# Optimization experiments

Hardware: AMD Instinct MI355X
Metric: run time of the kernel (lower is better)

Reference implementation:

```python
import jax, jax.numpy as jnp
import numpy as np

B, T, C, H = 8, 2048, 384, 64

def setup_inputs() -> dict:
    key = jax.random.key(0)
    k1, k2, k3, k4 = jax.random.split(key, 4)
    x = jax.random.normal(k1, (B, T, C), dtype=jnp.float32)
    Wq = jax.random.normal(k2, (C, H), dtype=jnp.float32) * (C ** -0.5)
    Wk = jax.random.normal(k3, (C, H), dtype=jnp.float32) * (C ** -0.5)
    Wv = jax.random.normal(k4, (C, H), dtype=jnp.float32) * (C ** -0.5)
    return {"x": x, "Wq": Wq, "Wk": Wk, "Wv": Wv}

def reference(x, Wq, Wk, Wv):
    # x: (B, T, C); projections: (B, T, H)
    Bn, Tn, Cn = x.shape
    q = jnp.einsum('btc,ch->bth', x, Wq)
    k = jnp.einsum('btc,ch->bth', x, Wk)
    v = jnp.einsum('btc,ch->bth', x, Wv)
    # NOTE: source scales by C**-0.5 (embedding dim), not head_size**-0.5
    weights = jnp.einsum('bth,bsh->bts', q, k) * (Cn ** -0.5)  # (B, T, T)
    causal = jnp.tril(jnp.ones((Tn, Tn), dtype=bool))
    weights = jnp.where(causal, weights, -jnp.inf)
    # NOTE: source applies softmax over dim=1 (query/row axis), reproduced faithfully
    weights = jax.nn.softmax(weights, axis=1)
    # dropout omitted (eval-mode reference)
    return jnp.einsum('bts,bsh->bth', weights, v)
```

## Files before the change

kernel.cpp:

```cpp
#include <hip/hip_runtime.h>
#include <hip/hip_bf16.h>
#include <math.h>

#define Bn 8
#define Tn 2048
#define Cn 384
#define Hn 64
#define SCALE 0.051031036307982884f

using bf16x8 = __attribute__((ext_vector_type(8))) short;
using f32x4  = __attribute__((ext_vector_type(4))) float;

#define MFMA(a, b, c) __builtin_amdgcn_mfma_f32_16x16x32_bf16((a), (b), (c), 0, 0, 0)

static __device__ __forceinline__ short f2bf(float f) {
  unsigned u = __float_as_uint(f);
  u += 0x7fffu + ((u >> 16) & 1u);
  return (short)(u >> 16);
}
static __device__ __forceinline__ float bf2f(short s) {
  return __uint_as_float(((unsigned)(unsigned short)s) << 16);
}

__global__ __launch_bounds__(256) void wconv_kernel(
    const float* __restrict__ Wq, const float* __restrict__ Wk,
    const float* __restrict__ Wv, short* __restrict__ WbT) {
  int idx = blockIdx.x * 256 + threadIdx.x;
  int n = idx / 384, k = idx - n * 384;
  const float* W = (n < 64) ? Wq : (n < 128) ? Wk : Wv;
  WbT[idx] = f2bf(W[k * 64 + (n & 63)]);
}

__global__ __launch_bounds__(256) void proj_kernel(
    const float* __restrict__ x, const short* __restrict__ WbT,
    short* __restrict__ qb, short* __restrict__ kb, short* __restrict__ vT) {
  __shared__ short xs[16][392];
  __shared__ short vtile[64][20];
  const int tid = threadIdx.x;
  const int t0 = blockIdx.x * 16;
  const float* xb = x + (size_t)t0 * Cn;
  #pragma unroll
  for (int i = 0; i < 6; ++i) {
    int j = tid + i * 256;
    int row = j / 96, colv = (j - row * 96) * 4;
    float4 v = *(const float4*)(xb + row * Cn + colv);
    short4 s4; s4.x = f2bf(v.x); s4.y = f2bf(v.y); s4.z = f2bf(v.z); s4.w = f2bf(v.w);
    *(short4*)(&xs[row][colv]) = s4;
  }
  __syncthreads();
  const int w = tid >> 6, l15 = tid & 15, quad = (tid & 63) >> 4;
  f32x4 acc[3] = {};
  for (int ks = 0; ks < 12; ++ks) {
    bf16x8 a = *(const bf16x8*)(&xs[l15][ks * 32 + quad * 8]);
    #pragma unroll
    for (int cf = 0; cf < 3; ++cf) {
      bf16x8 bfr = *(const bf16x8*)(WbT + (size_t)(48 * w + 16 * cf + l15) * Cn + ks * 32 + quad * 8);
      acc[cf] = MFMA(a, bfr, acc[cf]);
    }
  }
  #pragma unroll
  for (int cf = 0; cf < 3; ++cf) {
    int cbase = 48 * w + 16 * cf, c = cbase + l15;
    #pragma unroll
    for (int r = 0; r < 4; ++r) {
      int row = t0 + quad * 4 + r;
      short val = f2bf(acc[cf][r]);
      if (cbase < 64)       qb[(size_t)row * Hn + c] = val;
      else if (cbase < 128) kb[(size_t)row * Hn + (c - 64)] = val;
      else                  vtile[c - 128][quad * 4 + r] = val;
    }
  }
  __syncthreads();
  const int b = t0 >> 11, t0l = t0 & 2047;
  int h = tid >> 2, tseg = (tid & 3) * 4;
  *(short4*)(vT + ((size_t)(b * Hn + h)) * Tn + t0l + tseg) =
      *(const short4*)(&vtile[h][tseg]);
}

__global__ __launch_bounds__(256) void colstats_kernel(
    const short* __restrict__ qb, const short* __restrict__ kb,
    float* __restrict__ L, short* __restrict__ Eb) {
  const int unit = blockIdx.x;
  const int b = unit >> 7, rem = unit & 127;
  const int j = rem >> 3, u = rem & 7;
  const int lo = (u * 33) >> 3, hi = ((u + 1) * 33) >> 3;
  const int big = 32 - j;
  const int tid = threadIdx.x, w = tid >> 6, l15 = tid & 15, quad = (tid & 63) >> 4;
  const size_t Ebase = (size_t)b * Tn * Tn;
  __shared__ float redl[64][17];

  auto run = [&](const int i, const int k0, const int k1) {
    if (k0 >= k1) return;
    const int s0 = i << 6;
    bf16x8 bk[8];
    #pragma unroll
    for (int nf = 0; nf < 4; ++nf) {
      const size_t krow = (size_t)(b * Tn + s0 + 16 * nf + l15) * Hn;
      bk[2 * nf]     = *(const bf16x8*)(kb + krow + quad * 8);
      bk[2 * nf + 1] = *(const bf16x8*)(kb + krow + 32 + quad * 8);
    }
    float l[4] = {0.f, 0.f, 0.f, 0.f};
    auto cload = [&](bf16x8& A0, bf16x8& A1, int k) {
      size_t ar = (size_t)(b * Tn + ((i + k) << 6) + 16 * w + l15) * Hn;
      A0 = *(const bf16x8*)(qb + ar + quad * 8);
      A1 = *(const bf16x8*)(qb + ar + 32 + quad * 8);
    };
    auto ccomp = [&](bf16x8 A0, bf16x8 A1, int k) {
      f32x4 sc[4] = {};
      #pragma unroll
      for (int nf = 0; nf < 4; ++nf) {
        sc[nf] = MFMA(A0, bk[2 * nf], sc[nf]);
        sc[nf] = MFMA(A1, bk[2 * nf + 1], sc[nf]);
      }
      const bool diag = (k == 0);
      const int tb = ((i + k) << 6) + 16 * w + quad * 4;
      #pragma unroll
      for (int nf = 0; nf < 4; ++nf) {
        int s = s0 + 16 * nf + l15;
        #pragma unroll
        for (int r = 0; r < 4; ++r) {
          float v = sc[nf][r] * SCALE;
          if (diag && (tb + r) < s) v = -INFINITY;
          float ev = __expf(v);
          l[nf] += ev;
          Eb[Ebase + (size_t)(tb + r) * Tn + s] = f2bf(ev);
        }
      }
    };
    bf16x8 a0A, a1A, a0B, a1B;
    cload(a0A, a1A, k0);
    int k = k0;
    while (k + 1 < k1) {
      cload(a0B, a1B, k + 1);
      ccomp(a0A, a1A, k);
      if (k + 2 < k1) cload(a0A, a1A, k + 2);
      ccomp(a0B, a1B, k + 1);
      k += 2;
    }
    if (k < k1) ccomp(a0A, a1A, k);
    __syncthreads();
    #pragma unroll
    for (int nf = 0; nf < 4; ++nf) redl[16 * nf + l15][w * 4 + quad] = l[nf];
    __syncthreads();
    if (tid < 64) {
      float ls = 0.f;
      #pragma unroll
      for (int q2 = 0; q2 < 16; ++q2) ls += redl[tid][q2];
      atomicAdd(&L[b * Tn + s0 + tid], ls);
    }
  };
  run(j, lo, min(hi, big));
  run(31 - j, max(lo, big) - big, hi - big);
}

__global__ __launch_bounds__(256) void vhat_kernel(
    const short* __restrict__ vT, const float* __restrict__ L,
    short* __restrict__ vS) {
  int gid = blockIdx.x * 256 + threadIdx.x;
  size_t base = (size_t)gid * 8;
  int b = (int)(base >> 17), s = (int)(base & 2047);
  short4 v0 = *(const short4*)(vT + base);
  short4 v1 = *(const short4*)(vT + base + 4);
  const float* Lp = L + b * Tn + s;
  float4 L0 = *(const float4*)(Lp);
  float4 L1 = *(const float4*)(Lp + 4);
  short4 r0, r1;
  r0.x = f2bf(bf2f(v0.x) / L0.x); r0.y = f2bf(bf2f(v0.y) / L0.y);
  r0.z = f2bf(bf2f(v0.z) / L0.z); r0.w = f2bf(bf2f(v0.w) / L0.w);
  r1.x = f2bf(bf2f(v1.x) / L1.x); r1.y = f2bf(bf2f(v1.y) / L1.y);
  r1.z = f2bf(bf2f(v1.z) / L1.z); r1.w = f2bf(bf2f(v1.w) / L1.w);
  *(short4*)(vS + base) = r0;
  *(short4*)(vS + base + 4) = r1;
}

__global__ __launch_bounds__(256) void outg_kernel(
    const short* __restrict__ Eb, const short* __restrict__ vS,
    float* __restrict__ out) {
  const int unit = blockIdx.x;
  const int b = unit >> 7, rem = unit & 127;
  const int j = rem >> 3, u = rem & 7;
  const int lo = (u * 33) >> 3, hi = ((u + 1) * 33) >> 3;
  const int big = 32 - j;
  const int tid = threadIdx.x, w = tid >> 6, l15 = tid & 15, quad = (tid & 63) >> 4;
  const size_t Bbase = (size_t)b * Hn * Tn;

  auto run = [&](const int tile, const int k0, const int k1) {
    if (k0 >= k1) return;
    const int tbase = (tile << 6) + 16 * w;
    const size_t Abase = (size_t)b * Tn * Tn + (size_t)(tbase + l15) * Tn;
    f32x4 acc[4] = {};
    bf16x8 aA[2], bA[8], aB[2], bB[8];
    auto load = [&](bf16x8 (&A)[2], bf16x8 (&Bf)[8], int ch) {
      const int s0 = ch << 6;
      A[0] = *(const bf16x8*)(Eb + Abase + s0 + quad * 8);
      A[1] = *(const bf16x8*)(Eb + Abase + s0 + 32 + quad * 8);
      #pragma unroll
      for (int nf = 0; nf < 4; ++nf) {
        const size_t br = Bbase + (size_t)(16 * nf + l15) * Tn + s0;
        Bf[2 * nf]     = *(const bf16x8*)(vS + br + quad * 8);
        Bf[2 * nf + 1] = *(const bf16x8*)(vS + br + 32 + quad * 8);
      }
    };
    auto comp = [&](bf16x8 (&A)[2], bf16x8 (&Bf)[8]) {
      #pragma unroll
      for (int nf = 0; nf < 4; ++nf) {
        acc[nf] = MFMA(A[0], Bf[2 * nf], acc[nf]);
        acc[nf] = MFMA(A[1], Bf[2 * nf + 1], acc[nf]);
      }
    };
    load(aA, bA, k0);
    int ch = k0;
    while (ch + 1 < k1) {
      load(aB, bB, ch + 1);
      comp(aA, bA);
      if (ch + 2 < k1) load(aA, bA, ch + 2);
      comp(aB, bB);
      ch += 2;
    }
    if (ch < k1) comp(aA, bA);
    #pragma unroll
    for (int nf = 0; nf < 4; ++nf)
      #pragma unroll
      for (int r = 0; r < 4; ++r)
        atomicAdd(&out[(size_t)(b * Tn + tbase + quad * 4 + r) * Hn + 16 * nf + l15],
                  acc[nf][r]);
  };
  run(31 - j, lo, min(hi, big));
  run(j, max(lo, big) - big, hi - big);
}

extern "C" void kernel_launch(void* const* d_in, const int* in_sizes, int n_in,
                              void* d_out, int out_size, void* d_ws, size_t ws_size,
                              hipStream_t stream) {
  const float* x  = (const float*)d_in[0];
  const float* Wq = (const float*)d_in[1];
  const float* Wk = (const float*)d_in[2];
  const float* Wv = (const float*)d_in[3];
  char* ws = (char*)d_ws;
  short* qb   = (short*)(ws);
  short* kb   = (short*)(ws + 2097152);
  short* vT   = (short*)(ws + 4194304);
  short* vS   = (short*)(ws + 6291456);
  short* WbT  = (short*)(ws + 8388608);
  float* L    = (float*)(ws + 8536064);
  short* Eb   = (short*)(ws + 16777216);
  float* outp = (float*)d_out;

  hipMemsetAsync(L, 0, (size_t)Bn * Tn * 4, stream);
  hipMemsetAsync(outp, 0, (size_t)Bn * Tn * Hn * 4, stream);
  hipLaunchKernelGGL(wconv_kernel, dim3(288), dim3(256), 0, stream, Wq, Wk, Wv, WbT);
  hipLaunchKernelGGL(proj_kernel, dim3(Bn * Tn / 16), dim3(256), 0, stream, x, WbT, qb, kb, vT);
  hipLaunchKernelGGL(colstats_kernel, dim3(1024), dim3(256), 0, stream, qb, kb, L, Eb);
  hipLaunchKernelGGL(vhat_kernel, dim3(512), dim3(256), 0, stream, vT, L, vS);
  hipLaunchKernelGGL(outg_kernel, dim3(1024), dim3(256), 0, stream, Eb, vS, outp);
}
```

Before: 147.5 us.

## Replace atomic column sums with partial buffers and fold memsets into vhat

Result: no change. 144.8 us (-1.9%).

```diff
diff --git a/kernel.cpp b/kernel.cpp
--- a/kernel.cpp
+++ b/kernel.cpp
@@ -79,7 +79,7 @@
 
 __global__ __launch_bounds__(256) void colstats_kernel(
     const short* __restrict__ qb, const short* __restrict__ kb,
-    float* __restrict__ L, short* __restrict__ Eb) {
+    float* __restrict__ pL, short* __restrict__ Eb) {
   const int unit = blockIdx.x;
   const int b = unit >> 7, rem = unit & 127;
   const int j = rem >> 3, u = rem & 7;
@@ -89,55 +89,56 @@
   const size_t Ebase = (size_t)b * Tn * Tn;
   __shared__ float redl[64][17];
 
-  auto run = [&](const int i, const int k0, const int k1) {
-    if (k0 >= k1) return;
+  auto run = [&](const int i, const int k0, const int k1, const int slot) {
     const int s0 = i << 6;
-    bf16x8 bk[8];
-    #pragma unroll
-    for (int nf = 0; nf < 4; ++nf) {
-      const size_t krow = (size_t)(b * Tn + s0 + 16 * nf + l15) * Hn;
-      bk[2 * nf]     = *(const bf16x8*)(kb + krow + quad * 8);
-      bk[2 * nf + 1] = *(const bf16x8*)(kb + krow + 32 + quad * 8);
-    }
     float l[4] = {0.f, 0.f, 0.f, 0.f};
-    auto cload = [&](bf16x8& A0, bf16x8& A1, int k) {
-      size_t ar = (size_t)(b * Tn + ((i + k) << 6) + 16 * w + l15) * Hn;
-      A0 = *(const bf16x8*)(qb + ar + quad * 8);
-      A1 = *(const bf16x8*)(qb + ar + 32 + quad * 8);
-    };
-    auto ccomp = [&](bf16x8 A0, bf16x8 A1, int k) {
-      f32x4 sc[4] = {};
+    if (k0 < k1) {
+      bf16x8 bk[8];
       #pragma unroll
       for (int nf = 0; nf < 4; ++nf) {
-        sc[nf] = MFMA(A0, bk[2 * nf], sc[nf]);
-        sc[nf] = MFMA(A1, bk[2 * nf + 1], sc[nf]);
-      }
-      const bool diag = (k == 0);
-      const int tb = ((i + k) << 6) + 16 * w + quad * 4;
-      #pragma unroll
-      for (int nf = 0; nf < 4; ++nf) {
-        int s = s0 + 16 * nf + l15;
+        const size_t krow = (size_t)(b * Tn + s0 + 16 * nf + l15) * Hn;
+        bk[2 * nf]     = *(const bf16x8*)(kb + krow + quad * 8);
+        bk[2 * nf + 1] = *(const bf16x8*)(kb + krow + 32 + quad * 8);
+      }
+      auto cload = [&](bf16x8& A0, bf16x8& A1, int k) {
+        size_t ar = (size_t)(b * Tn + ((i + k) << 6) + 16 * w + l15) * Hn;
+        A0 = *(const bf16x8*)(qb + ar + quad * 8);
+        A1 = *(const bf16x8*)(qb + ar + 32 + quad * 8);
+      };
+      auto ccomp = [&](bf16x8 A0, bf16x8 A1, int k) {
+        f32x4 sc[4] = {};
         #pragma unroll
-        for (int r = 0; r < 4; ++r) {
-          float v = sc[nf][r] * SCALE;
-          if (diag && (tb + r) < s) v = -INFINITY;
-          float ev = __expf(v);
-          l[nf] += ev;
-          Eb[Ebase + (size_t)(tb + r) * Tn + s] = f2bf(ev);
+        for (int nf = 0; nf < 4; ++nf) {
+          sc[nf] = MFMA(A0, bk[2 * nf], sc[nf]);
+          sc[nf] = MFMA(A1, bk[2 * nf + 1], sc[nf]);
         }
-      }
-    };
-    bf16x8 a0A, a1A, a0B, a1B;
-    cload(a0A, a1A, k0);
-    int k = k0;
-    while (k + 1 < k1) {
-      cload(a0B, a1B, k + 1);
-      ccomp(a0A, a1A, k);
-      if (k + 2 < k1) cload(a0A, a1A, k + 2);
-      ccomp(a0B, a1B, k + 1);
-      k += 2;
-    }
-    if (k < k1) ccomp(a0A, a1A, k);
+        const bool diag = (k == 0);
+        const int tb = ((i + k) << 6) + 16 * w + quad * 4;
+        #pragma unroll
+        for (int nf = 0; nf < 4; ++nf) {
+          int s = s0 + 16 * nf + l15;
+          #pragma unroll
+          for (int r = 0; r < 4; ++r) {
+            float v = sc[nf][r] * SCALE;
+            if (diag && (tb + r) < s) v = -INFINITY;
+            float ev = __expf(v);
+            l[nf] += ev;
+            Eb[Ebase + (size_t)(tb + r) * Tn + s] = f2bf(ev);
+          }
+        }
+      };
+      bf16x8 a0A, a1A, a0B, a1B;
+      cload(a0A, a1A, k0);
+      int k = k0;
+      while (k + 1 < k1) {
+        cload(a0B, a1B, k + 1);
+        ccomp(a0A, a1A, k);
+        if (k + 2 < k1) cload(a0A, a1A, k + 2);
+        ccomp(a0B, a1B, k + 1);
+        k += 2;
+      }
+      if (k < k1) ccomp(a0A, a1A, k);
+    }
     __syncthreads();
     #pragma unroll
     for (int nf = 0; nf < 4; ++nf) redl[16 * nf + l15][w * 4 + quad] = l[nf];
@@ -146,31 +147,44 @@
       float ls = 0.f;
       #pragma unroll
       for (int q2 = 0; q2 < 16; ++q2) ls += redl[tid][q2];
-      atomicAdd(&L[b * Tn + s0 + tid], ls);
+      pL[unit * 128 + slot * 64 + tid] = ls;
     }
   };
-  run(j, lo, min(hi, big));
-  run(31 - j, max(lo, big) - big, hi - big);
+  run(j, lo, min(hi, big), 0);
+  run(31 - j, max(lo, big) - big, hi - big, 1);
 }
 
 __global__ __launch_bounds__(256) void vhat_kernel(
-    const short* __restrict__ vT, const float* __restrict__ L,
-    short* __restrict__ vS) {
+    const short* __restrict__ vT, const float* __restrict__ pL,
+    short* __restrict__ vS, float* __restrict__ outz) {
   int gid = blockIdx.x * 256 + threadIdx.x;
   size_t base = (size_t)gid * 8;
   int b = (int)(base >> 17), s = (int)(base & 2047);
+  int i = s >> 6, c = s & 63;
+  int j2 = (i < 16) ? i : 31 - i;
+  int slot = (i < 16) ? 0 : 1;
+  const float* pp = pL + (size_t)((b * 16 + j2) * 8) * 128 + slot * 64 + c;
+  float L0x = 0.f, L0y = 0.f, L0z = 0.f, L0w = 0.f;
+  float L1x = 0.f, L1y = 0.f, L1z = 0.f, L1w = 0.f;
+  #pragma unroll
+  for (int u = 0; u < 8; ++u) {
+    float4 p0 = *(const float4*)(pp + u * 128);
+    float4 p1 = *(const float4*)(pp + u * 128 + 4);
+    L0x += p0.x; L0y += p0.y; L0z += p0.z; L0w += p0.w;
+    L1x += p1.x; L1y += p1.y; L1z += p1.z; L1w += p1.w;
+  }
   short4 v0 = *(const short4*)(vT + base);
   short4 v1 = *(const short4*)(vT + base + 4);
-  const float* Lp = L + b * Tn + s;
-  float4 L0 = *(const float4*)(Lp);
-  float4 L1 = *(const float4*)(Lp + 4);
   short4 r0, r1;
-  r0.x = f2bf(bf2f(v0.x) / L0.x); r0.y = f2bf(bf2f(v0.y) / L0.y);
-  r0.z = f2bf(bf2f(v0.z) / L0.z); r0.w = f2bf(bf2f(v0.w) / L0.w);
-  r1.x = f2bf(bf2f(v1.x) / L1.x); r1.y = f2bf(bf2f(v1.y) / L1.y);
-  r1.z = f2bf(bf2f(v1.z) / L1.z); r1.w = f2bf(bf2f(v1.w) / L1.w);
+  r0.x = f2bf(bf2f(v0.x) / L0x); r0.y = f2bf(bf2f(v0.y) / L0y);
+  r0.z = f2bf(bf2f(v0.z) / L0z); r0.w = f2bf(bf2f(v0.w) / L0w);
+  r1.x = f2bf(bf2f(v1.x) / L1x); r1.y = f2bf(bf2f(v1.y) / L1y);
+  r1.z = f2bf(bf2f(v1.z) / L1z); r1.w = f2bf(bf2f(v1.w) / L1w);
   *(short4*)(vS + base) = r0;
   *(short4*)(vS + base + 4) = r1;
+  float4 z = {0.f, 0.f, 0.f, 0.f};
+  *(float4*)(outz + base) = z;
+  *(float4*)(outz + base + 4) = z;
 }
 
 __global__ __launch_bounds__(256) void outg_kernel(
@@ -242,15 +256,13 @@
   short* vT   = (short*)(ws + 4194304);
   short* vS   = (short*)(ws + 6291456);
   short* WbT  = (short*)(ws + 8388608);
-  float* L    = (float*)(ws + 8536064);
+  float* pL   = (float*)(ws + 8536064);
   short* Eb   = (short*)(ws + 16777216);
   float* outp = (float*)d_out;
 
-  hipMemsetAsync(L, 0, (size_t)Bn * Tn * 4, stream);
-  hipMemsetAsync(outp, 0, (size_t)Bn * Tn * Hn * 4, stream);
   hipLaunchKernelGGL(wconv_kernel, dim3(288), dim3(256), 0, stream, Wq, Wk, Wv, WbT);
   hipLaunchKernelGGL(proj_kernel, dim3(Bn * Tn / 16), dim3(256), 0, stream, x, WbT, qb, kb, vT);
-  hipLaunchKernelGGL(colstats_kernel, dim3(1024), dim3(256), 0, stream, qb, kb, L, Eb);
-  hipLaunchKernelGGL(vhat_kernel, dim3(512), dim3(256), 0, stream, vT, L, vS);
+  hipLaunchKernelGGL(colstats_kernel, dim3(1024), dim3(256), 0, stream, qb, kb, pL, Eb);
+  hipLaunchKernelGGL(vhat_kernel, dim3(512), dim3(256), 0, stream, vT, pL, vS, outp);
   hipLaunchKernelGGL(outg_kernel, dim3(1024), dim3(256), 0, stream, Eb, vS, outp);
 }
```
